# Kernel tuning notes

Measured on AMD Instinct MI355X. Metric: run time of the kernel, lower is better.

## Reference

```python
import jax, jax.numpy as jnp
import numpy as np

B, S, E, H = 4, 1024, 1024, 16
D = E // H
LN_EPS = 1e-5
W_SCALE = 0.02  # keep pre-softmax scores positive and moderate


def _linear(x, W, b):
    return x @ W + b


def _layernorm(x, g, b):
    m = jnp.mean(x, axis=-1, keepdims=True)
    v = jnp.mean((x - m) ** 2, axis=-1, keepdims=True)
    return (x - m) * jax.lax.rsqrt(v + LN_EPS) * g + b


def setup_inputs() -> dict:
    key = jax.random.key(0)
    ks = jax.random.split(key, 24)
    u = lambda k, shape, s=1.0: jax.random.uniform(k, shape, dtype=jnp.float32) * s
    inp = {
        'value': u(ks[0], (B, S, E)),
        'key':   u(ks[1], (B, S, E)),
        'query': u(ks[2], (B, S, E)),
        'mask':  jnp.ones((B, 1, 1, S), dtype=jnp.int32),
        # attention projections (W stored as [in, out])
        'Wv': u(ks[3], (E, E), W_SCALE), 'bv': u(ks[4], (E,), W_SCALE),
        'Wk': u(ks[5], (E, E), W_SCALE), 'bk': u(ks[6], (E,), W_SCALE),
        'Wq': u(ks[7], (E, E), W_SCALE), 'bq': u(ks[8], (E,), W_SCALE),
        'Wo': u(ks[9], (E, E), W_SCALE), 'bo': u(ks[10], (E,), W_SCALE),
        # feed-forward
        'W1': u(ks[11], (E, 4 * E), W_SCALE), 'b1': u(ks[12], (4 * E,), W_SCALE),
        'W2': u(ks[13], (4 * E, E), W_SCALE), 'b2': u(ks[14], (E,), W_SCALE),
        # layer norms
        'g1': jnp.ones((E,), jnp.float32), 'be1': jnp.zeros((E,), jnp.float32),
        'g2': jnp.ones((E,), jnp.float32), 'be2': jnp.zeros((E,), jnp.float32),
    }
    return inp


def reference(value, key, query, mask, Wv, bv, Wk, bk, Wq, bq, Wo, bo,
              W1, b1, W2, b2, g1, be1, g2, be2):
    b, q_len, _ = query.shape
    v = _linear(value, Wv, bv).reshape(b, -1, H, D)   # [B,K,H,D]
    k = _linear(key, Wk, bk).reshape(b, -1, H, D)     # [B,K,H,D]
    q = _linear(query, Wq, bq).reshape(b, q_len, H, D)
    att = jnp.einsum('bqhd,bkhd->bhqk', q, k)         # raw scores
    att = jnp.where(mask == 0, -jnp.inf, att)
    att = jnp.power(att, -0.5)                        # custom score^{-1/2} transform
    att = jax.nn.softmax(att, axis=3)
    ctx = jnp.einsum('bhqk,bkhd->bqhd', att, v).reshape(b, q_len, E)
    attn_out = _linear(ctx, Wo, bo)
    x = _layernorm(attn_out + query, g1, be1)         # dropout = identity (eval)
    ff = _linear(jax.nn.relu(_linear(x, W1, b1)), W2, b2)
    return _layernorm(ff + x, g2, be2)
```

## Files before the change

### kernel.cpp

```cpp
#include <hip/hip_runtime.h>
#include <hip/hip_bf16.h>
#include <cstdint>

typedef __hip_bfloat16 bf16;
typedef float f32x4 __attribute__((ext_vector_type(4)));
typedef short bf16x8 __attribute__((ext_vector_type(8)));
typedef short bf16x4v __attribute__((ext_vector_type(4)));

#define S_LEN 1024
#define EDIM  1024

__device__ __forceinline__ float bfs2f(short s) {
  return __uint_as_float(((unsigned)(unsigned short)s) << 16);
}
__device__ __forceinline__ short f2bfs(float f) {
  union { __hip_bfloat16 h; short s; } u;
  u.h = __float2bfloat16(f);
  return u.s;
}
__device__ __forceinline__ void glds16(const void* g, void* l) {
  __builtin_amdgcn_global_load_lds(
      (const __attribute__((address_space(1))) void*)g,
      (__attribute__((address_space(3))) void*)l, 16, 0, 0);
}
__device__ __forceinline__ bf16x8 cvt8(float4 a, float4 b) {
  bf16x8 w;
  w[0] = f2bfs(a.x); w[1] = f2bfs(a.y); w[2] = f2bfs(a.z); w[3] = f2bfs(a.w);
  w[4] = f2bfs(b.x); w[5] = f2bfs(b.y); w[6] = f2bfs(b.z); w[7] = f2bfs(b.w);
  return w;
}
__device__ __forceinline__ float score_xform(float s) {
  float r, e;
  asm("v_rsq_f32 %0, %1" : "=v"(r) : "v"(s));
  r *= 1.44269504088896f;
  asm("v_exp_f32 %0, %1" : "=v"(e) : "v"(r));
  return e;
}
__device__ __forceinline__ int xcd_swz(int bid, int nwg) {
  const int q = nwg >> 3, r = nwg & 7, xcd = bid & 7, j = bid >> 3;
  return (xcd < r ? xcd * (q + 1) : r * (q + 1) + (xcd - r) * q) + j;
}

struct Cvt3 { const float* in[3]; bf16* out[3]; };
__global__ __launch_bounds__(256)
void k_cvt3(Cvt3 p, int n4) {
  const float4* in = (const float4*)p.in[blockIdx.y];
  bf16x4v* out = (bf16x4v*)p.out[blockIdx.y];
  for (int i = blockIdx.x * 256 + threadIdx.x; i < n4; i += gridDim.x * 256) {
    float4 v = in[i];
    bf16x4v o;
    o[0] = f2bfs(v.x); o[1] = f2bfs(v.y); o[2] = f2bfs(v.z); o[3] = f2bfs(v.w);
    out[i] = o;
  }
}

struct TW4 { const float* in[4]; bf16* out[4]; };
__global__ void k_transpose_w4(TW4 p) {
  __shared__ bf16 t[32][33];
  const float* in = p.in[blockIdx.z];
  bf16* out = p.out[blockIdx.z];
  const int c0 = blockIdx.x * 32, r0 = blockIdx.y * 32;
  const int x = threadIdx.x;
  for (int yy = threadIdx.y; yy < 32; yy += 8)
    t[yy][x] = __float2bfloat16(in[(size_t)(r0 + yy) * 1024 + c0 + x]);
  __syncthreads();
  for (int yy = threadIdx.y; yy < 32; yy += 8)
    out[(size_t)(c0 + yy) * 1024 + r0 + x] = t[x][yy];
}

__global__ void k_transpose_w(const float* __restrict__ in, bf16* __restrict__ out,
                              int R, int C) {
  __shared__ bf16 t[32][33];
  const int c0 = blockIdx.x * 32, r0 = blockIdx.y * 32;
  const int x = threadIdx.x;
  for (int yy = threadIdx.y; yy < 32; yy += 8)
    t[yy][x] = __float2bfloat16(in[(size_t)(r0 + yy) * C + c0 + x]);
  __syncthreads();
  for (int yy = threadIdx.y; yy < 32; yy += 8)
    out[(size_t)(c0 + yy) * R + r0 + x] = t[x][yy];
}

__global__ void k_transpose_v(const bf16* __restrict__ v, bf16* __restrict__ vt) {
  __shared__ bf16 t[32][33];
  const int bh = blockIdx.z;
  const bf16* in = v + (size_t)(bh >> 4) * S_LEN * EDIM + (bh & 15) * 64;
  bf16* out = vt + (size_t)bh * 64 * S_LEN;
  const int d0 = blockIdx.x * 32, s0 = blockIdx.y * 32;
  const int x = threadIdx.x;
  for (int yy = threadIdx.y; yy < 32; yy += 8)
    t[yy][x] = in[(size_t)(s0 + yy) * EDIM + d0 + x];
  __syncthreads();
  for (int yy = threadIdx.y; yy < 32; yy += 8)
    out[(size_t)(d0 + yy) * S_LEN + s0 + x] = t[x][yy];
}

template <int RELU, int OUT_F32, int HAS_BIAS>
__device__ __forceinline__ void gemm_body(
    const bf16* __restrict__ A, int lda, const bf16* __restrict__ Bt, int ldb,
    const float* __restrict__ bias, void* __restrict__ Cout, int ldc,
    int K, int koff, int bm, int bn, bf16* lA, bf16* lB) {
  const int tid  = threadIdx.x;
  const int lane = tid & 63;
  const int wid  = tid >> 6;
  const int wm = wid >> 1, wn = wid & 1;
  const int fr = lane & 15, fg = lane >> 4;
  const int r0 = tid >> 2;
  const int c8 = (tid & 3) << 3;

  const bf16* Ag0 = A + (size_t)(bm + r0) * lda + koff + c8;
  const bf16* Ag1 = Ag0 + (size_t)64 * lda;
  const bf16* Bg0 = Bt + (size_t)(bn + r0) * ldb + koff + c8;
  const bf16* Bg1 = Bg0 + (size_t)64 * ldb;

  glds16(Ag0, (char*)lA + wid * 1024);
  glds16(Ag1, (char*)lA + wid * 1024 + 4096);
  glds16(Bg0, (char*)lB + wid * 1024);
  glds16(Bg1, (char*)lB + wid * 1024 + 4096);
  __syncthreads();

  f32x4 acc[4][4] = {};
  const int nt = K >> 5;
  int cur = 0;
  for (int t = 0; t < nt; t++) {
    const int kn = (t + 1) << 5;
    if (t + 1 < nt) {
      char* da = (char*)lA + (cur ^ 1) * 8192 + wid * 1024;
      char* db = (char*)lB + (cur ^ 1) * 8192 + wid * 1024;
      glds16(Ag0 + kn, da);
      glds16(Ag1 + kn, da + 4096);
      glds16(Bg0 + kn, db);
      glds16(Bg1 + kn, db + 4096);
    }
    const bf16* la = lA + cur * 4096;
    const bf16* lb = lB + cur * 4096;
    bf16x8 af[4], bv[4];
#pragma unroll
    for (int i = 0; i < 4; i++)
      af[i] = *(const bf16x8*)(la + (wm * 64 + i * 16 + fr) * 32 + fg * 8);
#pragma unroll
    for (int j = 0; j < 4; j++)
      bv[j] = *(const bf16x8*)(lb + (wn * 64 + j * 16 + fr) * 32 + fg * 8);
#pragma unroll
    for (int i = 0; i < 4; i++)
#pragma unroll
      for (int j = 0; j < 4; j++)
        acc[i][j] = __builtin_amdgcn_mfma_f32_16x16x32_bf16(af[i], bv[j], acc[i][j], 0, 0, 0);
    __syncthreads();
    cur ^= 1;
  }

  float bvals[4];
#pragma unroll
  for (int j = 0; j < 4; j++)
    bvals[j] = HAS_BIAS ? bias[bn + wn * 64 + j * 16 + fr] : 0.f;
#pragma unroll
  for (int i = 0; i < 4; i++) {
    const size_t orow = bm + wm * 64 + i * 16 + fg * 4;
#pragma unroll
    for (int r = 0; r < 4; r++) {
#pragma unroll
      for (int j = 0; j < 4; j++) {
        float v = acc[i][j][r] + bvals[j];
        if (RELU) v = fmaxf(v, 0.f);
        const size_t idx = (orow + r) * (size_t)ldc + bn + wn * 64 + j * 16 + fr;
        if (OUT_F32) ((float*)Cout)[idx] = v;
        else ((bf16*)Cout)[idx] = __float2bfloat16(v);
      }
    }
  }
}

template <int RELU, int OUT_F32, int SPLITK>
__global__ __launch_bounds__(256)
void k_gemm_bt(const bf16* __restrict__ A, int lda, const bf16* __restrict__ Bt,
               int ldb, const float* __restrict__ bias, void* __restrict__ Cout,
               int ldc, int K, size_t zstr) {
  __shared__ __align__(16) bf16 lA[2 * 4096];
  __shared__ __align__(16) bf16 lB[2 * 4096];
  const int nwg = gridDim.x * gridDim.y;
  int bid = xcd_swz(blockIdx.y * gridDim.x + blockIdx.x, nwg);
  const int bx = bid % gridDim.x, by = bid / gridDim.x;
  int koff = 0;
  void* Co = Cout;
  if (SPLITK) {
    koff = blockIdx.z * K;
    Co = (float*)Cout + (size_t)blockIdx.z * zstr;
  }
  gemm_body<RELU, OUT_F32, !SPLITK>(A, lda, Bt, ldb, bias, Co, ldc,
                                    K, koff, by * 128, bx * 128, lA, lB);
}

struct QkvPtrs { const bf16* A[3]; const bf16* B[3]; const float* bias[3]; bf16* C[3]; };
__global__ __launch_bounds__(256)
void k_gemm_qkv(QkvPtrs p) {
  __shared__ __align__(16) bf16 lA[2 * 4096];
  __shared__ __align__(16) bf16 lB[2 * 4096];
  const int nwg = gridDim.x * gridDim.y;
  int bid = xcd_swz(blockIdx.y * gridDim.x + blockIdx.x, nwg);
  const int bx = bid % gridDim.x;
  int by = bid / gridDim.x;
  const int grp = by >> 5;
  by &= 31;
  gemm_body<0, 0, 1>(p.A[grp], 1024, p.B[grp], 1024, p.bias[grp], p.C[grp],
                     1024, 1024, 0, by * 128, bx * 128, lA, lB);
}

__global__ __launch_bounds__(256)
void k_attn(const bf16* __restrict__ q, const bf16* __restrict__ k,
            const bf16* __restrict__ vt, bf16* __restrict__ ctx) {
  const int qt = blockIdx.x;
  const int bh = blockIdx.y;
  const int b = bh >> 4, h = bh & 15;
  const int tid = threadIdx.x, lane = tid & 63, w = tid >> 6;
  const int fr = lane & 15, fg = lane >> 4;
  const bf16* Q  = q  + (size_t)b * S_LEN * EDIM + h * 64;
  const bf16* Kp = k  + (size_t)b * S_LEN * EDIM + h * 64;
  const bf16* V  = vt + (size_t)bh * 64 * S_LEN;

  __shared__ __align__(16) bf16 lK[2][64 * 64];
  __shared__ __align__(16) bf16 lV[2][64 * 64];
  __shared__ __align__(16) bf16 eL[4][32][72];

  const int srow = lane >> 3;
  const int scol = (((lane & 7) ^ srow) << 3);
  const int rsw  = (fr & 7) << 3;

  bf16x8 qf[2][2];
#pragma unroll
  for (int i = 0; i < 2; i++)
#pragma unroll
    for (int ks = 0; ks < 2; ks++)
      qf[i][ks] = *(const bf16x8*)(Q + (size_t)(qt * 128 + w * 32 + i * 16 + fr) * EDIM + ks * 32 + fg * 8);

#pragma unroll
  for (int c = 0; c < 2; c++) {
    const int r = w * 8 + c * 32 + srow;
    glds16(Kp + (size_t)r * EDIM + scol, (char*)&lK[0][(w * 8 + c * 32) * 64]);
    glds16(V + (size_t)r * S_LEN + scol, (char*)&lV[0][(w * 8 + c * 32) * 64]);
  }
  __syncthreads();

  f32x4 accO[2][4] = {};
  float lsum[2][4] = {};
  int cur = 0;
  for (int kt = 0; kt < S_LEN; kt += 64) {
    if (kt + 64 < S_LEN) {
#pragma unroll
      for (int c = 0; c < 2; c++) {
        const int r = w * 8 + c * 32 + srow;
        glds16(Kp + (size_t)(kt + 64 + r) * EDIM + scol,
               (char*)&lK[cur ^ 1][(w * 8 + c * 32) * 64]);
        glds16(V + (size_t)r * S_LEN + kt + 64 + scol,
               (char*)&lV[cur ^ 1][(w * 8 + c * 32) * 64]);
      }
    }
    f32x4 accS[2][4] = {};
#pragma unroll
    for (int ks = 0; ks < 2; ks++)
#pragma unroll
      for (int j = 0; j < 4; j++) {
        bf16x8 kf = *(const bf16x8*)(&lK[cur][(j * 16 + fr) * 64 + ((ks * 32 + fg * 8) ^ rsw)]);
#pragma unroll
        for (int i = 0; i < 2; i++)
          accS[i][j] = __builtin_amdgcn_mfma_f32_16x16x32_bf16(qf[i][ks], kf, accS[i][j], 0, 0, 0);
      }
#pragma unroll
    for (int i = 0; i < 2; i++)
#pragma unroll
      for (int j = 0; j < 4; j++)
#pragma unroll
        for (int r = 0; r < 4; r++) {
          float p = score_xform(accS[i][j][r]);
          lsum[i][r] += p;
          eL[w][i * 16 + fg * 4 + r][j * 16 + fr] = __float2bfloat16(p);
        }
#pragma unroll
    for (int ks = 0; ks < 2; ks++) {
      bf16x8 af[2];
#pragma unroll
      for (int i = 0; i < 2; i++)
        af[i] = *(const bf16x8*)(&eL[w][i * 16 + fr][ks * 32 + fg * 8]);
#pragma unroll
      for (int j = 0; j < 4; j++) {
        bf16x8 vf = *(const bf16x8*)(&lV[cur][(j * 16 + fr) * 64 + ((ks * 32 + fg * 8) ^ rsw)]);
#pragma unroll
        for (int i = 0; i < 2; i++)
          accO[i][j] = __builtin_amdgcn_mfma_f32_16x16x32_bf16(af[i], vf, accO[i][j], 0, 0, 0);
      }
    }
    __syncthreads();
    cur ^= 1;
  }

#pragma unroll
  for (int i = 0; i < 2; i++)
#pragma unroll
    for (int r = 0; r < 4; r++) {
      float s = lsum[i][r];
      s += __shfl_xor(s, 1, 64);
      s += __shfl_xor(s, 2, 64);
      s += __shfl_xor(s, 4, 64);
      s += __shfl_xor(s, 8, 64);
      lsum[i][r] = s;
    }
#pragma unroll
  for (int i = 0; i < 2; i++)
#pragma unroll
    for (int r = 0; r < 4; r++) {
      const size_t qrow = (size_t)qt * 128 + w * 32 + i * 16 + fg * 4 + r;
      const float inv = 1.0f / lsum[i][r];
#pragma unroll
      for (int j = 0; j < 4; j++)
        ctx[((size_t)b * S_LEN + qrow) * EDIM + h * 64 + j * 16 + fr] =
            __float2bfloat16(accO[i][j][r] * inv);
    }
}

template <int A_F32, int RES_F32, int OUT_F32>
__global__ __launch_bounds__(256)
void k_ln_res(const void* __restrict__ a_, const void* __restrict__ res_,
              const float* __restrict__ g, const float* __restrict__ be,
              void* __restrict__ out_) {
  const int row = blockIdx.x;
  const int tid = threadIdx.x;
  const int lane = tid & 63, wid = tid >> 6;
  const size_t base = (size_t)row * EDIM + tid * 4;
  float x[4];
  if (A_F32) {
    float4 v = *(const float4*)((const float*)a_ + base);
    x[0] = v.x; x[1] = v.y; x[2] = v.z; x[3] = v.w;
  } else {
    bf16x4v v = *(const bf16x4v*)((const bf16*)a_ + base);
#pragma unroll
    for (int i = 0; i < 4; i++) x[i] = bfs2f(v[i]);
  }
  if (RES_F32) {
    float4 v = *(const float4*)((const float*)res_ + base);
    x[0] += v.x; x[1] += v.y; x[2] += v.z; x[3] += v.w;
  } else {
    bf16x4v v = *(const bf16x4v*)((const bf16*)res_ + base);
#pragma unroll
    for (int i = 0; i < 4; i++) x[i] += bfs2f(v[i]);
  }

  float s = x[0] + x[1] + x[2] + x[3];
#pragma unroll
  for (int o = 32; o >= 1; o >>= 1) s += __shfl_xor(s, o, 64);
  __shared__ float red[4], red2[4];
  if (lane == 0) red[wid] = s;
  __syncthreads();
  const float mean = (red[0] + red[1] + red[2] + red[3]) * (1.0f / 1024.0f);

  float d[4], s2 = 0.f;
#pragma unroll
  for (int i = 0; i < 4; i++) { d[i] = x[i] - mean; s2 += d[i] * d[i]; }
#pragma unroll
  for (int o = 32; o >= 1; o >>= 1) s2 += __shfl_xor(s2, o, 64);
  if (lane == 0) red2[wid] = s2;
  __syncthreads();
  const float var = (red2[0] + red2[1] + red2[2] + red2[3]) * (1.0f / 1024.0f);
  const float inv = rsqrtf(var + 1e-5f);

  float4 g4 = *(const float4*)(g + tid * 4);
  float4 b4 = *(const float4*)(be + tid * 4);
  float o0 = d[0] * inv * g4.x + b4.x;
  float o1 = d[1] * inv * g4.y + b4.y;
  float o2 = d[2] * inv * g4.z + b4.z;
  float o3 = d[3] * inv * g4.w + b4.w;
  if (OUT_F32) {
    *(float4*)((float*)out_ + base) = make_float4(o0, o1, o2, o3);
  } else {
    bf16x4v o;
    o[0] = f2bfs(o0); o[1] = f2bfs(o1); o[2] = f2bfs(o2); o[3] = f2bfs(o3);
    *(bf16x4v*)((bf16*)out_ + base) = o;
  }
}

template <int RES_F32, int OUT_F32>
__global__ __launch_bounds__(256)
void k_ln_res2(const float* __restrict__ p0, const float* __restrict__ p1,
               const float* __restrict__ bias, const void* __restrict__ res_,
               const float* __restrict__ g, const float* __restrict__ be,
               void* __restrict__ out_) {
  const int row = blockIdx.x;
  const int tid = threadIdx.x;
  const int lane = tid & 63, wid = tid >> 6;
  const size_t base = (size_t)row * EDIM + tid * 4;
  float4 a = *(const float4*)(p0 + base);
  float4 b = *(const float4*)(p1 + base);
  float4 c = *(const float4*)(bias + tid * 4);
  float x[4];
  x[0] = a.x + b.x + c.x;
  x[1] = a.y + b.y + c.y;
  x[2] = a.z + b.z + c.z;
  x[3] = a.w + b.w + c.w;
  if (RES_F32) {
    float4 v = *(const float4*)((const float*)res_ + base);
    x[0] += v.x; x[1] += v.y; x[2] += v.z; x[3] += v.w;
  } else {
    bf16x4v v = *(const bf16x4v*)((const bf16*)res_ + base);
#pragma unroll
    for (int i = 0; i < 4; i++) x[i] += bfs2f(v[i]);
  }

  float s = x[0] + x[1] + x[2] + x[3];
#pragma unroll
  for (int o = 32; o >= 1; o >>= 1) s += __shfl_xor(s, o, 64);
  __shared__ float red[4], red2[4];
  if (lane == 0) red[wid] = s;
  __syncthreads();
  const float mean = (red[0] + red[1] + red[2] + red[3]) * (1.0f / 1024.0f);

  float d[4], s2 = 0.f;
#pragma unroll
  for (int i = 0; i < 4; i++) { d[i] = x[i] - mean; s2 += d[i] * d[i]; }
#pragma unroll
  for (int o = 32; o >= 1; o >>= 1) s2 += __shfl_xor(s2, o, 64);
  if (lane == 0) red2[wid] = s2;
  __syncthreads();
  const float var = (red2[0] + red2[1] + red2[2] + red2[3]) * (1.0f / 1024.0f);
  const float inv = rsqrtf(var + 1e-5f);

  float4 g4 = *(const float4*)(g + tid * 4);
  float4 b4 = *(const float4*)(be + tid * 4);
  float o0 = d[0] * inv * g4.x + b4.x;
  float o1 = d[1] * inv * g4.y + b4.y;
  float o2 = d[2] * inv * g4.z + b4.z;
  float o3 = d[3] * inv * g4.w + b4.w;
  if (OUT_F32) {
    *(float4*)((float*)out_ + base) = make_float4(o0, o1, o2, o3);
  } else {
    bf16x4v o;
    o[0] = f2bfs(o0); o[1] = f2bfs(o1); o[2] = f2bfs(o2); o[3] = f2bfs(o3);
    *(bf16x4v*)((bf16*)out_ + base) = o;
  }
}

extern "C" void kernel_launch(void* const* d_in, const int* in_sizes, int n_in,
                              void* d_out, int out_size, void* d_ws, size_t ws_size,
                              hipStream_t stream) {
  const float* value = (const float*)d_in[0];
  const float* key_  = (const float*)d_in[1];
  const float* query = (const float*)d_in[2];
  const float* Wv = (const float*)d_in[4];  const float* bv = (const float*)d_in[5];
  const float* Wk = (const float*)d_in[6];  const float* bk = (const float*)d_in[7];
  const float* Wq = (const float*)d_in[8];  const float* bq = (const float*)d_in[9];
  const float* Wo = (const float*)d_in[10]; const float* bo = (const float*)d_in[11];
  const float* W1 = (const float*)d_in[12]; const float* b1 = (const float*)d_in[13];
  const float* W2 = (const float*)d_in[14]; const float* b2 = (const float*)d_in[15];
  const float* g1 = (const float*)d_in[16]; const float* be1 = (const float*)d_in[17];
  const float* g2 = (const float*)d_in[18]; const float* be2 = (const float*)d_in[19];

  bf16* ws = (bf16*)d_ws;
  const size_t MEG = 1024 * 1024;
  bf16* WqT = ws + 0 * MEG;
  bf16* WkT = ws + 1 * MEG;
  bf16* WvT = ws + 2 * MEG;
  bf16* WoT = ws + 3 * MEG;
  bf16* W1T = ws + 4 * MEG;
  bf16* W2T = ws + 8 * MEG;
  bf16* qx  = ws + 12 * MEG;
  bf16* kx  = ws + 16 * MEG;
  bf16* vx  = ws + 20 * MEG;
  bf16* qb  = ws + 24 * MEG;
  bf16* kb  = ws + 28 * MEG;
  bf16* vb  = ws + 32 * MEG;
  bf16* vtb = ws + 36 * MEG;
  bf16* ctx = ws + 12 * MEG;
  float* p0w = (float*)(ws + 16 * MEG);
  float* p1w = (float*)(ws + 24 * MEG);
  const size_t zstrW = 4 * MEG;
  bf16* xb  = ws + 36 * MEG;
  bf16* h1  = ws + 12 * MEG;
  float* f0 = (float*)ws;
  float* f1 = (float*)(ws + 28 * MEG);
  const size_t zstrF = 14 * MEG;

  const dim3 tb(32, 8);
  Cvt3 cp;
  cp.in[0] = query; cp.out[0] = qx;
  cp.in[1] = key_;  cp.out[1] = kx;
  cp.in[2] = value; cp.out[2] = vx;
  k_cvt3<<<dim3(1024, 3), 256, 0, stream>>>(cp, 1024 * 1024);

  TW4 tw;
  tw.in[0] = Wq; tw.out[0] = WqT;
  tw.in[1] = Wk; tw.out[1] = WkT;
  tw.in[2] = Wv; tw.out[2] = WvT;
  tw.in[3] = Wo; tw.out[3] = WoT;
  k_transpose_w4<<<dim3(32, 32, 4), tb, 0, stream>>>(tw);
  k_transpose_w<<<dim3(128, 32), tb, 0, stream>>>(W1, W1T, 1024, 4096);
  k_transpose_w<<<dim3(32, 128), tb, 0, stream>>>(W2, W2T, 4096, 1024);

  QkvPtrs qp;
  qp.A[0] = qx; qp.B[0] = WqT; qp.bias[0] = bq; qp.C[0] = qb;
  qp.A[1] = kx; qp.B[1] = WkT; qp.bias[1] = bk; qp.C[1] = kb;
  qp.A[2] = vx; qp.B[2] = WvT; qp.bias[2] = bv; qp.C[2] = vb;
  k_gemm_qkv<<<dim3(8, 96), 256, 0, stream>>>(qp);

  k_transpose_v<<<dim3(2, 32, 64), tb, 0, stream>>>(vb, vtb);
  k_attn<<<dim3(8, 64), 256, 0, stream>>>(qb, kb, vtb, ctx);

  k_gemm_bt<0, 1, 1><<<dim3(8, 32, 2), 256, 0, stream>>>(
      ctx, 1024, WoT, 1024, nullptr, p0w, 1024, 512, zstrW);
  k_ln_res2<1, 0><<<4096, 256, 0, stream>>>(p0w, p1w, bo, query, g1, be1, xb);

  k_gemm_bt<1, 0, 0><<<dim3(32, 32), 256, 0, stream>>>(
      xb, 1024, W1T, 1024, b1, h1, 4096, 1024, 0);
  k_gemm_bt<0, 1, 1><<<dim3(8, 32, 2), 256, 0, stream>>>(
      h1, 4096, W2T, 4096, nullptr, f0, 1024, 2048, zstrF);
  k_ln_res2<0, 1><<<4096, 256, 0, stream>>>(f0, f1, b2, xb, g2, be2, (float*)d_out);
}
```

Before: 257.2 us.

## Replace 128x128 GEMMs with 256x256 8-wave pipelined GEMM kernel

Replaces the 128x128-tile, 4-wave double-buffered bf16 GEMM with a 256x256-tile, 512-thread kernel. It uses 64-wide K steps, XOR-swizzled LDS staging, staggered A/B prefetch interleaved between four MFMA quadrants, and s_setprio around the MFMA blocks. The aim is higher arithmetic intensity per LDS byte and better overlap of global loads with MFMA work. The FFN2 split-K grows to 4 partials when the workspace allows, and the LN kernel is generalized to sum N partials. In exchange each block needs 128KB of shared memory, and the grids are small (e.g. 64-128 blocks for the QKV/Wo GEMMs), which risks underfilling the CUs.

Result: faster. 233.3 us (median of 4 runs) (-9.3%).

```diff
diff --git a/kernel.cpp b/kernel.cpp
--- a/kernel.cpp
+++ b/kernel.cpp
@@ -22,12 +22,6 @@
   __builtin_amdgcn_global_load_lds(
       (const __attribute__((address_space(1))) void*)g,
       (__attribute__((address_space(3))) void*)l, 16, 0, 0);
-}
-__device__ __forceinline__ bf16x8 cvt8(float4 a, float4 b) {
-  bf16x8 w;
-  w[0] = f2bfs(a.x); w[1] = f2bfs(a.y); w[2] = f2bfs(a.z); w[3] = f2bfs(a.w);
-  w[4] = f2bfs(b.x); w[5] = f2bfs(b.y); w[6] = f2bfs(b.z); w[7] = f2bfs(b.w);
-  return w;
 }
 __device__ __forceinline__ float score_xform(float s) {
   float r, e;
@@ -40,6 +34,8 @@
   const int q = nwg >> 3, r = nwg & 7, xcd = bid & 7, j = bid >> 3;
   return (xcd < r ? xcd * (q + 1) : r * (q + 1) + (xcd - r) * q) + j;
 }
+#define BAR() do { __builtin_amdgcn_s_barrier(); asm volatile("" ::: "memory"); } while (0)
+#define WAITV(n) asm volatile("s_waitcnt vmcnt(" #n ")" ::: "memory")
 
 struct Cvt3 { const float* in[3]; bf16* out[3]; };
 __global__ __launch_bounds__(256)
@@ -95,74 +91,147 @@
 }
 
 template <int RELU, int OUT_F32, int HAS_BIAS>
-__device__ __forceinline__ void gemm_body(
+__device__ __forceinline__ void gemm8_body(
     const bf16* __restrict__ A, int lda, const bf16* __restrict__ Bt, int ldb,
     const float* __restrict__ bias, void* __restrict__ Cout, int ldc,
-    int K, int koff, int bm, int bn, bf16* lA, bf16* lB) {
-  const int tid  = threadIdx.x;
-  const int lane = tid & 63;
-  const int wid  = tid >> 6;
-  const int wm = wid >> 1, wn = wid & 1;
+    int K, int koff, int bm, int bn, char* smem) {
+  const int tid = threadIdx.x, lane = tid & 63, wid = tid >> 6;
+  const int wm = wid >> 2;
+  const int wn = wid & 3;
   const int fr = lane & 15, fg = lane >> 4;
-  const int r0 = tid >> 2;
-  const int c8 = (tid & 3) << 3;
-
-  const bf16* Ag0 = A + (size_t)(bm + r0) * lda + koff + c8;
-  const bf16* Ag1 = Ag0 + (size_t)64 * lda;
-  const bf16* Bg0 = Bt + (size_t)(bn + r0) * ldb + koff + c8;
-  const bf16* Bg1 = Bg0 + (size_t)64 * ldb;
-
-  glds16(Ag0, (char*)lA + wid * 1024);
-  glds16(Ag1, (char*)lA + wid * 1024 + 4096);
-  glds16(Bg0, (char*)lB + wid * 1024);
-  glds16(Bg1, (char*)lB + wid * 1024 + 4096);
-  __syncthreads();
-
-  f32x4 acc[4][4] = {};
-  const int nt = K >> 5;
-  int cur = 0;
-  for (int t = 0; t < nt; t++) {
-    const int kn = (t + 1) << 5;
-    if (t + 1 < nt) {
-      char* da = (char*)lA + (cur ^ 1) * 8192 + wid * 1024;
-      char* db = (char*)lB + (cur ^ 1) * 8192 + wid * 1024;
-      glds16(Ag0 + kn, da);
-      glds16(Ag1 + kn, da + 4096);
-      glds16(Bg0 + kn, db);
-      glds16(Bg1 + kn, db + 4096);
-    }
-    const bf16* la = lA + cur * 4096;
-    const bf16* lb = lB + cur * 4096;
-    bf16x8 af[4], bv[4];
+  const int sw = (fr & 7) << 4;
+
+  const int rr = lane >> 3;
+  const int cc = ((lane & 7) ^ rr) << 3;
+
+  #define STG(src, ld, dstoff)                                                  \
+    {                                                                           \
+      const bf16* _s = (src);                                                   \
+      _Pragma("unroll")                                                         \
+      for (int _j = 0; _j < 2; _j++) {                                          \
+        const int _L = wid * 2 + _j;                                            \
+        glds16(_s + (size_t)(_L * 8 + rr) * (ld) + cc, smem + (dstoff) + _L * 1024); \
+      }                                                                         \
+    }
+
+  const bf16* Abase = A + (size_t)bm * lda + koff;
+  const bf16* Bbase = Bt + (size_t)bn * ldb + koff;
+  const int nt = K >> 6;
+
+  STG(Abase + cc * 0, lda, 0);
+  STG(Abase + (size_t)128 * lda, lda, 16384);
+  STG(Bbase, ldb, 32768);
+  STG(Bbase + (size_t)128 * ldb, ldb, 49152);
+  if (nt > 1) {
+    STG(Bbase + 64, ldb, 65536 + 32768);
+    STG(Bbase + (size_t)128 * ldb + 64, ldb, 65536 + 49152);
+  }
+  WAITV(0);
+  BAR();
+
+  f32x4 acc[8][4] = {};
+  bf16x8 af[4][2], b01[2][2], b23[2][2];
+
+  const int aRd = wm * 16384 + fr * 128;
+  const int bRd = 32768 + (wn >> 1) * 16384 + (wn & 1) * 8192 + fr * 128;
+  const int c0s = (0 * 64 + fg * 16) ^ sw;
+  const int c1s = (1 * 64 + fg * 16) ^ sw;
+
+  for (int n = 0; n < nt; n++) {
+    const int buf = (n & 1) << 16;
+    const int nbuf = buf ^ 65536;
+    const char* sb = smem + buf;
+    const int kA = (n + 1) << 6;
+    const int kB = (n + 2) << 6;
+
+#pragma unroll
+    for (int i = 0; i < 4; i++) {
+      af[i][0] = *(const bf16x8*)(sb + aRd + i * 2048 + c0s);
+      af[i][1] = *(const bf16x8*)(sb + aRd + i * 2048 + c1s);
+    }
+#pragma unroll
+    for (int j = 0; j < 2; j++) {
+      b01[j][0] = *(const bf16x8*)(sb + bRd + j * 2048 + c0s);
+      b01[j][1] = *(const bf16x8*)(sb + bRd + j * 2048 + c1s);
+    }
+    if (n + 1 < nt) STG(Abase + kA, lda, nbuf);
+    BAR();
+    __builtin_amdgcn_s_setprio(1);
 #pragma unroll
     for (int i = 0; i < 4; i++)
-      af[i] = *(const bf16x8*)(la + (wm * 64 + i * 16 + fr) * 32 + fg * 8);
-#pragma unroll
-    for (int j = 0; j < 4; j++)
-      bv[j] = *(const bf16x8*)(lb + (wn * 64 + j * 16 + fr) * 32 + fg * 8);
+#pragma unroll
+      for (int j = 0; j < 2; j++) {
+        acc[i][j] = __builtin_amdgcn_mfma_f32_16x16x32_bf16(af[i][0], b01[j][0], acc[i][j], 0, 0, 0);
+        acc[i][j] = __builtin_amdgcn_mfma_f32_16x16x32_bf16(af[i][1], b01[j][1], acc[i][j], 0, 0, 0);
+      }
+    __builtin_amdgcn_s_setprio(0);
+    BAR();
+
+#pragma unroll
+    for (int j = 0; j < 2; j++) {
+      b23[j][0] = *(const bf16x8*)(sb + bRd + (j + 2) * 2048 + c0s);
+      b23[j][1] = *(const bf16x8*)(sb + bRd + (j + 2) * 2048 + c1s);
+    }
+    if (n + 1 < nt) STG(Abase + (size_t)128 * lda + kA, lda, nbuf + 16384);
+    BAR();
+    __builtin_amdgcn_s_setprio(1);
 #pragma unroll
     for (int i = 0; i < 4; i++)
 #pragma unroll
-      for (int j = 0; j < 4; j++)
-        acc[i][j] = __builtin_amdgcn_mfma_f32_16x16x32_bf16(af[i], bv[j], acc[i][j], 0, 0, 0);
-    __syncthreads();
-    cur ^= 1;
-  }
-
-  float bvals[4];
+      for (int j = 0; j < 2; j++) {
+        acc[i][j + 2] = __builtin_amdgcn_mfma_f32_16x16x32_bf16(af[i][0], b23[j][0], acc[i][j + 2], 0, 0, 0);
+        acc[i][j + 2] = __builtin_amdgcn_mfma_f32_16x16x32_bf16(af[i][1], b23[j][1], acc[i][j + 2], 0, 0, 0);
+      }
+    __builtin_amdgcn_s_setprio(0);
+    BAR();
+
+#pragma unroll
+    for (int i = 0; i < 4; i++) {
+      af[i][0] = *(const bf16x8*)(sb + aRd + (i + 4) * 2048 + c0s);
+      af[i][1] = *(const bf16x8*)(sb + aRd + (i + 4) * 2048 + c1s);
+    }
+    if (n + 2 < nt) STG(Bbase + kB, ldb, buf + 32768);
+    BAR();
+    __builtin_amdgcn_s_setprio(1);
+#pragma unroll
+    for (int i = 0; i < 4; i++)
+#pragma unroll
+      for (int j = 0; j < 2; j++) {
+        acc[i + 4][j + 2] = __builtin_amdgcn_mfma_f32_16x16x32_bf16(af[i][0], b23[j][0], acc[i + 4][j + 2], 0, 0, 0);
+        acc[i + 4][j + 2] = __builtin_amdgcn_mfma_f32_16x16x32_bf16(af[i][1], b23[j][1], acc[i + 4][j + 2], 0, 0, 0);
+      }
+    __builtin_amdgcn_s_setprio(0);
+    BAR();
+
+    if (n + 2 < nt) STG(Bbase + (size_t)128 * ldb + kB, ldb, buf + 49152);
+    __builtin_amdgcn_s_setprio(1);
+#pragma unroll
+    for (int i = 0; i < 4; i++)
+#pragma unroll
+      for (int j = 0; j < 2; j++) {
+        acc[i + 4][j] = __builtin_amdgcn_mfma_f32_16x16x32_bf16(af[i][0], b01[j][0], acc[i + 4][j], 0, 0, 0);
+        acc[i + 4][j] = __builtin_amdgcn_mfma_f32_16x16x32_bf16(af[i][1], b01[j][1], acc[i + 4][j], 0, 0, 0);
+      }
+    __builtin_amdgcn_s_setprio(0);
+    if (n + 2 < nt) { WAITV(4); } else { WAITV(0); }
+    BAR();
+  }
+  #undef STG
+
+  float bv4[4];
 #pragma unroll
   for (int j = 0; j < 4; j++)
-    bvals[j] = HAS_BIAS ? bias[bn + wn * 64 + j * 16 + fr] : 0.f;
-#pragma unroll
-  for (int i = 0; i < 4; i++) {
-    const size_t orow = bm + wm * 64 + i * 16 + fg * 4;
+    bv4[j] = HAS_BIAS ? bias[bn + wn * 64 + j * 16 + fr] : 0.f;
+#pragma unroll
+  for (int i = 0; i < 8; i++) {
+    const size_t rowb = (size_t)bm + wm * 128 + i * 16 + fg * 4;
 #pragma unroll
     for (int r = 0; r < 4; r++) {
 #pragma unroll
       for (int j = 0; j < 4; j++) {
-        float v = acc[i][j][r] + bvals[j];
+        float v = acc[i][j][r] + bv4[j];
         if (RELU) v = fmaxf(v, 0.f);
-        const size_t idx = (orow + r) * (size_t)ldc + bn + wn * 64 + j * 16 + fr;
+        const size_t idx = (rowb + r) * (size_t)ldc + bn + wn * 64 + j * 16 + fr;
         if (OUT_F32) ((float*)Cout)[idx] = v;
         else ((bf16*)Cout)[idx] = __float2bfloat16(v);
       }
@@ -170,39 +239,34 @@
   }
 }
 
-template <int RELU, int OUT_F32, int SPLITK>
-__global__ __launch_bounds__(256)
-void k_gemm_bt(const bf16* __restrict__ A, int lda, const bf16* __restrict__ Bt,
-               int ldb, const float* __restrict__ bias, void* __restrict__ Cout,
-               int ldc, int K, size_t zstr) {
-  __shared__ __align__(16) bf16 lA[2 * 4096];
-  __shared__ __align__(16) bf16 lB[2 * 4096];
+struct G8Args {
+  const bf16* A; int lda; const bf16* Bt; int ldb; const float* bias;
+  void* C[4]; int ldc; int Kz;
+};
+template <int RELU, int OUT_F32, int HAS_BIAS>
+__global__ __launch_bounds__(512, 2)
+void k_gemm8(G8Args a) {
+  __shared__ __align__(16) char smem[131072];
   const int nwg = gridDim.x * gridDim.y;
-  int bid = xcd_swz(blockIdx.y * gridDim.x + blockIdx.x, nwg);
+  const int bid = xcd_swz(blockIdx.y * gridDim.x + blockIdx.x, nwg);
   const int bx = bid % gridDim.x, by = bid / gridDim.x;
-  int koff = 0;
-  void* Co = Cout;
-  if (SPLITK) {
-    koff = blockIdx.z * K;
-    Co = (float*)Cout + (size_t)blockIdx.z * zstr;
-  }
-  gemm_body<RELU, OUT_F32, !SPLITK>(A, lda, Bt, ldb, bias, Co, ldc,
-                                    K, koff, by * 128, bx * 128, lA, lB);
-}
-
-struct QkvPtrs { const bf16* A[3]; const bf16* B[3]; const float* bias[3]; bf16* C[3]; };
-__global__ __launch_bounds__(256)
-void k_gemm_qkv(QkvPtrs p) {
-  __shared__ __align__(16) bf16 lA[2 * 4096];
-  __shared__ __align__(16) bf16 lB[2 * 4096];
+  gemm8_body<RELU, OUT_F32, HAS_BIAS>(
+      a.A, a.lda, a.Bt, a.ldb, a.bias, a.C[blockIdx.z], a.ldc,
+      a.Kz, blockIdx.z * a.Kz, by * 256, bx * 256, smem);
+}
+
+struct QkvArgs { const bf16* A[3]; const bf16* B[3]; const float* bias[3]; bf16* C[3]; };
+__global__ __launch_bounds__(512, 2)
+void k_gemm8_qkv(QkvArgs p) {
+  __shared__ __align__(16) char smem[131072];
   const int nwg = gridDim.x * gridDim.y;
-  int bid = xcd_swz(blockIdx.y * gridDim.x + blockIdx.x, nwg);
-  const int bx = bid % gridDim.x;
-  int by = bid / gridDim.x;
-  const int grp = by >> 5;
-  by &= 31;
-  gemm_body<0, 0, 1>(p.A[grp], 1024, p.B[grp], 1024, p.bias[grp], p.C[grp],
-                     1024, 1024, 0, by * 128, bx * 128, lA, lB);
+  const int bid = xcd_swz(blockIdx.y * gridDim.x + blockIdx.x, nwg);
+  const int bx = bid % (int)gridDim.x;
+  int by = bid / (int)gridDim.x;
+  const int grp = by >> 4;
+  by &= 15;
+  gemm8_body<0, 0, 1>(p.A[grp], 1024, p.B[grp], 1024, p.bias[grp],
+                      (void*)p.C[grp], 1024, 1024, 0, by * 256, bx * 256, smem);
 }
 
 __global__ __launch_bounds__(256)
@@ -316,84 +380,23 @@
     }
 }
 
-template <int A_F32, int RES_F32, int OUT_F32>
+struct LnP { const float* p[4]; };
+template <int NP, int RES_F32, int OUT_F32>
 __global__ __launch_bounds__(256)
-void k_ln_res(const void* __restrict__ a_, const void* __restrict__ res_,
-              const float* __restrict__ g, const float* __restrict__ be,
-              void* __restrict__ out_) {
+void k_ln_resN(LnP pp, const float* __restrict__ bias, const void* res_,
+               const float* __restrict__ g, const float* __restrict__ be,
+               void* out_) {
   const int row = blockIdx.x;
   const int tid = threadIdx.x;
   const int lane = tid & 63, wid = tid >> 6;
   const size_t base = (size_t)row * EDIM + tid * 4;
-  float x[4];
-  if (A_F32) {
-    float4 v = *(const float4*)((const float*)a_ + base);
-    x[0] = v.x; x[1] = v.y; x[2] = v.z; x[3] = v.w;
-  } else {
-    bf16x4v v = *(const bf16x4v*)((const bf16*)a_ + base);
-#pragma unroll
-    for (int i = 0; i < 4; i++) x[i] = bfs2f(v[i]);
-  }
-  if (RES_F32) {
-    float4 v = *(const float4*)((const float*)res_ + base);
+  float4 c = *(const float4*)(bias + tid * 4);
+  float x[4] = {c.x, c.y, c.z, c.w};
+#pragma unroll
+  for (int t = 0; t < NP; t++) {
+    float4 v = *(const float4*)(pp.p[t] + base);
     x[0] += v.x; x[1] += v.y; x[2] += v.z; x[3] += v.w;
-  } else {
-    bf16x4v v = *(const bf16x4v*)((const bf16*)res_ + base);
-#pragma unroll
-    for (int i = 0; i < 4; i++) x[i] += bfs2f(v[i]);
-  }
-
-  float s = x[0] + x[1] + x[2] + x[3];
-#pragma unroll
-  for (int o = 32; o >= 1; o >>= 1) s += __shfl_xor(s, o, 64);
-  __shared__ float red[4], red2[4];
-  if (lane == 0) red[wid] = s;
-  __syncthreads();
-  const float mean = (red[0] + red[1] + red[2] + red[3]) * (1.0f / 1024.0f);
-
-  float d[4], s2 = 0.f;
-#pragma unroll
-  for (int i = 0; i < 4; i++) { d[i] = x[i] - mean; s2 += d[i] * d[i]; }
-#pragma unroll
-  for (int o = 32; o >= 1; o >>= 1) s2 += __shfl_xor(s2, o, 64);
-  if (lane == 0) red2[wid] = s2;
-  __syncthreads();
-  const float var = (red2[0] + red2[1] + red2[2] + red2[3]) * (1.0f / 1024.0f);
-  const float inv = rsqrtf(var + 1e-5f);
-
-  float4 g4 = *(const float4*)(g + tid * 4);
-  float4 b4 = *(const float4*)(be + tid * 4);
-  float o0 = d[0] * inv * g4.x + b4.x;
-  float o1 = d[1] * inv * g4.y + b4.y;
-  float o2 = d[2] * inv * g4.z + b4.z;
-  float o3 = d[3] * inv * g4.w + b4.w;
-  if (OUT_F32) {
-    *(float4*)((float*)out_ + base) = make_float4(o0, o1, o2, o3);
-  } else {
-    bf16x4v o;
-    o[0] = f2bfs(o0); o[1] = f2bfs(o1); o[2] = f2bfs(o2); o[3] = f2bfs(o3);
-    *(bf16x4v*)((bf16*)out_ + base) = o;
-  }
-}
-
-template <int RES_F32, int OUT_F32>
-__global__ __launch_bounds__(256)
-void k_ln_res2(const float* __restrict__ p0, const float* __restrict__ p1,
-               const float* __restrict__ bias, const void* __restrict__ res_,
-               const float* __restrict__ g, const float* __restrict__ be,
-               void* __restrict__ out_) {
-  const int row = blockIdx.x;
-  const int tid = threadIdx.x;
-  const int lane = tid & 63, wid = tid >> 6;
-  const size_t base = (size_t)row * EDIM + tid * 4;
-  float4 a = *(const float4*)(p0 + base);
-  float4 b = *(const float4*)(p1 + base);
-  float4 c = *(const float4*)(bias + tid * 4);
-  float x[4];
-  x[0] = a.x + b.x + c.x;
-  x[1] = a.y + b.y + c.y;
-  x[2] = a.z + b.z + c.z;
-  x[3] = a.w + b.w + c.w;
+  }
   if (RES_F32) {
     float4 v = *(const float4*)((const float*)res_ + base);
     x[0] += v.x; x[1] += v.y; x[2] += v.z; x[3] += v.w;
@@ -451,30 +454,30 @@
   const float* g1 = (const float*)d_in[16]; const float* be1 = (const float*)d_in[17];
   const float* g2 = (const float*)d_in[18]; const float* be2 = (const float*)d_in[19];
 
-  bf16* ws = (bf16*)d_ws;
-  const size_t MEG = 1024 * 1024;
-  bf16* WqT = ws + 0 * MEG;
-  bf16* WkT = ws + 1 * MEG;
-  bf16* WvT = ws + 2 * MEG;
-  bf16* WoT = ws + 3 * MEG;
-  bf16* W1T = ws + 4 * MEG;
-  bf16* W2T = ws + 8 * MEG;
-  bf16* qx  = ws + 12 * MEG;
-  bf16* kx  = ws + 16 * MEG;
-  bf16* vx  = ws + 20 * MEG;
-  bf16* qb  = ws + 24 * MEG;
-  bf16* kb  = ws + 28 * MEG;
-  bf16* vb  = ws + 32 * MEG;
-  bf16* vtb = ws + 36 * MEG;
-  bf16* ctx = ws + 12 * MEG;
-  float* p0w = (float*)(ws + 16 * MEG);
-  float* p1w = (float*)(ws + 24 * MEG);
-  const size_t zstrW = 4 * MEG;
-  bf16* xb  = ws + 36 * MEG;
-  bf16* h1  = ws + 12 * MEG;
-  float* f0 = (float*)ws;
-  float* f1 = (float*)(ws + 28 * MEG);
-  const size_t zstrF = 14 * MEG;
+  char* wsb = (char*)d_ws;
+  const size_t MB = 1024 * 1024;
+  bf16* W1T = (bf16*)(wsb + 0 * MB);
+  bf16* W2T = (bf16*)(wsb + 8 * MB);
+  bf16* WqT = (bf16*)(wsb + 16 * MB);
+  bf16* WkT = (bf16*)(wsb + 18 * MB);
+  bf16* WvT = (bf16*)(wsb + 20 * MB);
+  bf16* WoT = (bf16*)(wsb + 22 * MB);
+  bf16* qx  = (bf16*)(wsb + 24 * MB);
+  bf16* kx  = (bf16*)(wsb + 32 * MB);
+  bf16* vx  = (bf16*)(wsb + 40 * MB);
+  bf16* qb  = (bf16*)(wsb + 48 * MB);
+  bf16* kb  = (bf16*)(wsb + 56 * MB);
+  bf16* vb  = (bf16*)(wsb + 64 * MB);
+  bf16* vtb = (bf16*)(wsb + 72 * MB);
+  bf16* ctx = (bf16*)(wsb + 24 * MB);
+  float* p0w = (float*)(wsb + 32 * MB);
+  float* p1w = (float*)(wsb + 48 * MB);
+  bf16* xb  = (bf16*)(wsb + 16 * MB);
+  bf16* h1  = (bf16*)(wsb + 24 * MB);
+  float* f1 = (float*)(wsb + 56 * MB);
+  float* f2 = (float*)(wsb + 72 * MB);
+  float* f3 = (float*)(wsb + 88 * MB);
+  const int splitF = (ws_size >= 108 * MB) ? 4 : 2;
 
   const dim3 tb(32, 8);
   Cvt3 cp;
@@ -492,22 +495,39 @@
   k_transpose_w<<<dim3(128, 32), tb, 0, stream>>>(W1, W1T, 1024, 4096);
   k_transpose_w<<<dim3(32, 128), tb, 0, stream>>>(W2, W2T, 4096, 1024);
 
-  QkvPtrs qp;
+  QkvArgs qp;
   qp.A[0] = qx; qp.B[0] = WqT; qp.bias[0] = bq; qp.C[0] = qb;
   qp.A[1] = kx; qp.B[1] = WkT; qp.bias[1] = bk; qp.C[1] = kb;
   qp.A[2] = vx; qp.B[2] = WvT; qp.bias[2] = bv; qp.C[2] = vb;
-  k_gemm_qkv<<<dim3(8, 96), 256, 0, stream>>>(qp);
+  k_gemm8_qkv<<<dim3(4, 48), 512, 0, stream>>>(qp);
 
   k_transpose_v<<<dim3(2, 32, 64), tb, 0, stream>>>(vb, vtb);
   k_attn<<<dim3(8, 64), 256, 0, stream>>>(qb, kb, vtb, ctx);
 
-  k_gemm_bt<0, 1, 1><<<dim3(8, 32, 2), 256, 0, stream>>>(
-      ctx, 1024, WoT, 1024, nullptr, p0w, 1024, 512, zstrW);
-  k_ln_res2<1, 0><<<4096, 256, 0, stream>>>(p0w, p1w, bo, query, g1, be1, xb);
-
-  k_gemm_bt<1, 0, 0><<<dim3(32, 32), 256, 0, stream>>>(
-      xb, 1024, W1T, 1024, b1, h1, 4096, 1024, 0);
-  k_gemm_bt<0, 1, 1><<<dim3(8, 32, 2), 256, 0, stream>>>(
-      h1, 4096, W2T, 4096, nullptr, f0, 1024, 2048, zstrF);
-  k_ln_res2<0, 1><<<4096, 256, 0, stream>>>(f0, f1, b2, xb, g2, be2, (float*)d_out);
-}
+  G8Args wo;
+  wo.A = ctx; wo.lda = 1024; wo.Bt = WoT; wo.ldb = 1024; wo.bias = nullptr;
+  wo.C[0] = p0w; wo.C[1] = p1w; wo.C[2] = nullptr; wo.C[3] = nullptr;
+  wo.ldc = 1024; wo.Kz = 512;
+  k_gemm8<0, 1, 0><<<dim3(4, 16, 2), 512, 0, stream>>>(wo);
+  LnP l1; l1.p[0] = p0w; l1.p[1] = p1w; l1.p[2] = nullptr; l1.p[3] = nullptr;
+  k_ln_resN<2, 1, 0><<<4096, 256, 0, stream>>>(l1, bo, query, g1, be1, xb);
+
+  G8Args ff1;
+  ff1.A = xb; ff1.lda = 1024; ff1.Bt = W1T; ff1.ldb = 1024; ff1.bias = b1;
+  ff1.C[0] = h1; ff1.C[1] = nullptr; ff1.C[2] = nullptr; ff1.C[3] = nullptr;
+  ff1.ldc = 4096; ff1.Kz = 1024;
+  k_gemm8<1, 0, 1><<<dim3(16, 16, 1), 512, 0, stream>>>(ff1);
+
+  G8Args ff2;
+  ff2.A = h1; ff2.lda = 4096; ff2.Bt = W2T; ff2.ldb = 4096; ff2.bias = nullptr;
+  ff2.C[0] = d_out; ff2.C[1] = f1; ff2.C[2] = f2; ff2.C[3] = f3;
+  ff2.ldc = 1024; ff2.Kz = 4096 / splitF;
+  k_gemm8<0, 1, 0><<<dim3(4, 16, splitF), 512, 0, stream>>>(ff2);
+
+  LnP l2;
+  l2.p[0] = (const float*)d_out; l2.p[1] = f1; l2.p[2] = f2; l2.p[3] = f3;
+  if (splitF == 4)
+    k_ln_resN<4, 0, 1><<<4096, 256, 0, stream>>>(l2, b2, xb, g2, be2, (float*)d_out);
+  else
+    k_ln_resN<2, 0, 1><<<4096, 256, 0, stream>>>(l2, b2, xb, g2, be2, (float*)d_out);
+}
```
